# Kernel optimization log

Measured on AMD Instinct MI355X. Metric: run time of the kernel, lower is better.

## Reference

```python
import jax, jax.numpy as jnp
import numpy as np

N_NODES = 100000
N_EDGES = 1600000
NODE_F = 64
EDGE_F = 32
BN_EPS = 1e-5


def setup_inputs() -> dict:
    key = jax.random.key(0)
    ks = jax.random.split(key, 8)
    in_dim = 2 * NODE_F + EDGE_F  # 160
    scale = 1.0 / np.sqrt(in_dim)
    return {
        "node_attrs": jax.random.normal(ks[0], (N_NODES, NODE_F), jnp.float32),
        "edge_index": jax.random.randint(ks[1], (2, N_EDGES), 0, N_NODES, jnp.int64),
        "edge_attrs": jax.random.normal(ks[2], (N_EDGES, EDGE_F), jnp.float32),
        "W_f": jax.random.normal(ks[3], (in_dim, NODE_F), jnp.float32) * scale,
        "b_f": jnp.zeros((NODE_F,), jnp.float32),
        "W_s": jax.random.normal(ks[4], (in_dim, NODE_F), jnp.float32) * scale,
        "b_s": jnp.zeros((NODE_F,), jnp.float32),
        "gamma": jnp.ones((NODE_F,), jnp.float32),
        "beta": jnp.zeros((NODE_F,), jnp.float32),
    }


def reference(node_attrs, edge_index, edge_attrs, W_f, b_f, W_s, b_s, gamma, beta):
    source, target = edge_index[0], edge_index[1]
    x_i = node_attrs[source]            # [E, F] gather
    x_j = node_attrs[target]            # [E, F] gather
    z = jnp.concatenate([x_i, x_j, edge_attrs], axis=-1)  # [E, 2F+Fe]
    # gated MLP: sigmoid(lin_f(z)) * softplus(lin_s(z))
    h = jax.nn.sigmoid(z @ W_f + b_f) * jax.nn.softplus(z @ W_s + b_s)  # [E, F]
    # scatter-add messages to source nodes
    message = jax.ops.segment_sum(h, source, num_segments=node_attrs.shape[0])  # [N, F]
    # BatchNorm1d in training mode: batch stats over node dim (biased variance)
    mean = jnp.mean(message, axis=0)
    var = jnp.mean((message - mean) ** 2, axis=0)
    normed = (message - mean) * jax.lax.rsqrt(var + BN_EPS) * gamma + beta
    return node_attrs + normed
```

## Files before the change

### kernel.cpp

```cpp
#include <hip/hip_runtime.h>
#include <math.h>

#define N_NODES 100000
#define N_EDGES 1600000
#define NODE_F  64
#define IN_DIM  160
#define N_TILES 25000
#define ZSTRIDE 168
#define EDGE_GRID 1792

typedef __attribute__((ext_vector_type(8))) short short8;
typedef __attribute__((ext_vector_type(4))) float f32x4;

static __device__ inline unsigned short f2bf(float f) {
    union { float f; unsigned u; } v; v.f = f;
    unsigned r = v.u + 0x7fffu + ((v.u >> 16) & 1u);
    return (unsigned short)(r >> 16);
}

static __device__ inline unsigned pack2(float lo, float hi) {
    union { float f; unsigned u; } a, b; a.f = lo; b.f = hi;
    const unsigned ra = a.u + 0x7fffu + ((a.u >> 16) & 1u);
    const unsigned rb = b.u + 0x7fffu + ((b.u >> 16) & 1u);
    return __builtin_amdgcn_perm(rb, ra, 0x07060302u);
}

static __device__ __forceinline__ void tile_barrier() {
    __builtin_amdgcn_sched_barrier(0);
    asm volatile("s_waitcnt lgkmcnt(0)" ::: "memory");
    __builtin_amdgcn_s_barrier();
    __builtin_amdgcn_sched_barrier(0);
}

__global__ __launch_bounds__(256, 7) void edge_kernel(
    const float* __restrict__ node_attrs,
    const int*   __restrict__ edge_src,
    const int*   __restrict__ edge_tgt,
    const float* __restrict__ edge_attrs,
    const float* __restrict__ W_f, const float* __restrict__ b_f,
    const float* __restrict__ W_s, const float* __restrict__ b_s,
    float* __restrict__ msg)
{
    __shared__ __align__(16) short sbuf[64 * ZSTRIDE];
    unsigned* sbuf32 = (unsigned*)sbuf;

    const int tid  = threadIdx.x;
    const int wave = tid >> 6;
    const int lane = tid & 63;
    const int quad = lane >> 4;
    const int l15  = lane & 15;

    short8 bF[5], bS[5];
#pragma unroll
    for (int mat = 0; mat < 2; ++mat) {
        const float* W = mat ? W_s : W_f;
        __syncthreads();
        for (int idx = tid; idx < IN_DIM * 64; idx += 256) {
            const int k = idx >> 6, n = idx & 63;
            sbuf[n * ZSTRIDE + k] = (short)f2bf(W[idx]);
        }
        __syncthreads();
#pragma unroll
        for (int kc = 0; kc < 5; ++kc) {
            const short8 b = *(const short8*)&sbuf[(16 * wave + l15) * ZSTRIDE + kc * 32 + quad * 8];
            if (mat) bS[kc] = b; else bF[kc] = b;
        }
    }

    const float bias_f = b_f[16 * wave + l15];
    const float bias_s = b_s[16 * wave + l15];
    float* const msgf  = msg + 16 * wave + l15;

    int srcv = edge_src[blockIdx.x * 64 + lane];
    int tgtv = edge_tgt[blockIdx.x * 64 + lane];

    for (int t = blockIdx.x; t < N_TILES; t += EDGE_GRID) {
        const int e0 = t * 64;

        tile_barrier();

#pragma unroll
        for (int i = 0; i < 8; ++i) {
            const int el   = i * 2 + (quad >> 1);
            const int half = quad & 1;
            const int sl   = 16 * wave + el;
            const int ns   = __shfl(srcv, sl);
            const int nt   = __shfl(tgtv, sl);
            const int node = half ? nt : ns;
            const float4 v = *(const float4*)&node_attrs[node * 64 + l15 * 4];
            uint2 o; o.x = pack2(v.x, v.y); o.y = pack2(v.z, v.w);
            *(uint2*)&sbuf32[sl * (ZSTRIDE / 2) + half * 32 + l15 * 2] = o;
        }
#pragma unroll
        for (int i = 0; i < 2; ++i) {
            const int p  = i * 256 + tid;
            const int el = p >> 3, g = p & 7;
            const float4 v = *(const float4*)&edge_attrs[(size_t)(e0 + el) * 32 + g * 4];
            uint2 o; o.x = pack2(v.x, v.y); o.y = pack2(v.z, v.w);
            *(uint2*)&sbuf32[el * (ZSTRIDE / 2) + 64 + g * 2] = o;
        }

        const int tn = t + EDGE_GRID;
        int nsrc = 0, ntgt = 0;
        if (tn < N_TILES) {
            nsrc = edge_src[tn * 64 + lane];
            ntgt = edge_tgt[tn * 64 + lane];
        }
        tile_barrier();

#pragma unroll
        for (int mt = 0; mt < 4; ++mt) {
            f32x4 accF = {0.f, 0.f, 0.f, 0.f};
            f32x4 accS = {0.f, 0.f, 0.f, 0.f};
#pragma unroll
            for (int kc = 0; kc < 5; ++kc) {
                const short8 a = *(const short8*)&sbuf[(mt * 16 + l15) * ZSTRIDE + kc * 32 + quad * 8];
                accF = __builtin_amdgcn_mfma_f32_16x16x32_bf16(a, bF[kc], accF, 0, 0, 0);
                accS = __builtin_amdgcn_mfma_f32_16x16x32_bf16(a, bS[kc], accS, 0, 0, 0);
            }
#pragma unroll
            for (int r = 0; r < 4; ++r) {
                const float xf = accF[r] + bias_f;
                const float xs = accS[r] + bias_s;
                const float sig = __builtin_amdgcn_rcpf(1.0f + __expf(-xf));
                const float sp  = fmaxf(xs, 0.0f) + __logf(1.0f + __expf(-fabsf(xs)));
                const float h   = sig * sp;
                const int sl    = mt * 16 + quad * 4 + r;
                const int node  = __shfl(srcv, sl);
                atomicAdd(&msgf[node * 64], h);
            }
        }

        srcv = nsrc;
        tgtv = ntgt;
    }
}

#define STATS_BLOCKS 1024
__global__ __launch_bounds__(256) void stats_kernel(
    const float* __restrict__ msg, float* __restrict__ stats)
{
    const int tid = threadIdx.x;
    const int g4  = tid & 15;
    const int r0  = tid >> 4;
    float4 s = {0.f, 0.f, 0.f, 0.f};
    float4 q = {0.f, 0.f, 0.f, 0.f};
    for (int r = blockIdx.x * 16 + r0; r < N_NODES; r += STATS_BLOCKS * 16) {
        const float4 v = *(const float4*)&msg[(size_t)r * 64 + g4 * 4];
        s.x += v.x; s.y += v.y; s.z += v.z; s.w += v.w;
        q.x = fmaf(v.x, v.x, q.x);
        q.y = fmaf(v.y, v.y, q.y);
        q.z = fmaf(v.z, v.z, q.z);
        q.w = fmaf(v.w, v.w, q.w);
    }
    __shared__ float4 rs[256];
    __shared__ float4 rq[256];
    rs[tid] = s;
    rq[tid] = q;
    __syncthreads();
    if (tid < 16) {
        float4 S = rs[tid];
        float4 Q = rq[tid];
        for (int k = 1; k < 16; ++k) {
            const float4 a = rs[k * 16 + tid];
            const float4 b = rq[k * 16 + tid];
            S.x += a.x; S.y += a.y; S.z += a.z; S.w += a.w;
            Q.x += b.x; Q.y += b.y; Q.z += b.z; Q.w += b.w;
        }
        atomicAdd(&stats[tid * 4 + 0], S.x);
        atomicAdd(&stats[tid * 4 + 1], S.y);
        atomicAdd(&stats[tid * 4 + 2], S.z);
        atomicAdd(&stats[tid * 4 + 3], S.w);
        atomicAdd(&stats[64 + tid * 4 + 0], Q.x);
        atomicAdd(&stats[64 + tid * 4 + 1], Q.y);
        atomicAdd(&stats[64 + tid * 4 + 2], Q.z);
        atomicAdd(&stats[64 + tid * 4 + 3], Q.w);
    }
}

__global__ __launch_bounds__(256) void norm_kernel(
    const float* __restrict__ node_attrs,
    const float* __restrict__ stats,
    const float* __restrict__ gamma,
    const float* __restrict__ beta,
    float* __restrict__ out)
{
    const int i = blockIdx.x * blockDim.x + threadIdx.x;
    const int idx = i * 4;
    if (idx >= N_NODES * 64) return;
    const int f = idx & 63;
    const float inv_n = 1.0f / (float)N_NODES;

    const float4 m4 = *(const float4*)&out[idx];
    const float4 x4 = *(const float4*)&node_attrs[idx];

    float mean[4], rstd[4], gm[4], bt[4];
#pragma unroll
    for (int j = 0; j < 4; ++j) {
        mean[j] = stats[f + j] * inv_n;
        const float var = stats[64 + f + j] * inv_n - mean[j] * mean[j];
        rstd[j] = rsqrtf(var + 1e-5f);
        gm[j] = gamma[f + j];
        bt[j] = beta[f + j];
    }
    float4 o;
    o.x = x4.x + (m4.x - mean[0]) * rstd[0] * gm[0] + bt[0];
    o.y = x4.y + (m4.y - mean[1]) * rstd[1] * gm[1] + bt[1];
    o.z = x4.z + (m4.z - mean[2]) * rstd[2] * gm[2] + bt[2];
    o.w = x4.w + (m4.w - mean[3]) * rstd[3] * gm[3] + bt[3];
    *(float4*)&out[idx] = o;
}

extern "C" void kernel_launch(void* const* d_in, const int* in_sizes, int n_in,
                              void* d_out, int out_size, void* d_ws, size_t ws_size,
                              hipStream_t stream)
{
    const float* node_attrs = (const float*)d_in[0];
    const int*   edge_index = (const int*)d_in[1];
    const float* edge_attrs = (const float*)d_in[2];
    const float* W_f   = (const float*)d_in[3];
    const float* b_f   = (const float*)d_in[4];
    const float* W_s   = (const float*)d_in[5];
    const float* b_s   = (const float*)d_in[6];
    const float* gamma = (const float*)d_in[7];
    const float* beta  = (const float*)d_in[8];

    float* out   = (float*)d_out;
    float* stats = (float*)d_ws;

    const int* edge_src = edge_index;
    const int* edge_tgt = edge_index + N_EDGES;

    hipMemsetAsync(out, 0, (size_t)N_NODES * NODE_F * sizeof(float), stream);
    hipMemsetAsync(stats, 0, 128 * sizeof(float), stream);

    edge_kernel<<<EDGE_GRID, 256, 0, stream>>>(
        node_attrs, edge_src, edge_tgt, edge_attrs, W_f, b_f, W_s, b_s, out);

    stats_kernel<<<STATS_BLOCKS, 256, 0, stream>>>(out, stats);

    norm_kernel<<<(N_NODES * NODE_F / 4 + 255) / 256, 256, 0, stream>>>(
        node_attrs, stats, gamma, beta, out);
}
```

Before: 718.9 us.

## Fuse edge, stats and norm kernels into one persistent kernel with grid barriers

Merges the three kernels into a single persistent launch of 1536 blocks that uses atomic-counter grid barriers between the scatter, batch-stats and normalization phases. The aim is to remove launch gaps and the separate stats memset. The grid shrinks from 1792 to 1536 blocks with a launch-bounds occupancy of 6, and the custom LDS-only barrier is replaced by plain __syncthreads. The grid barrier needs every block to be resident at once and has a spin-timeout fallback, so it risks wrong results or stalls if residency is not guaranteed. The barriers also serialize the tail work.

```diff
diff --git a/kernel.cpp b/kernel.cpp
--- a/kernel.cpp
+++ b/kernel.cpp
@@ -7,7 +7,8 @@
 #define IN_DIM  160
 #define N_TILES 25000
 #define ZSTRIDE 168
-#define EDGE_GRID 1792
+#define GRID    1536
+#define BLOCK   256
 
 typedef __attribute__((ext_vector_type(8))) short short8;
 typedef __attribute__((ext_vector_type(4))) float f32x4;
@@ -25,21 +26,33 @@
     return __builtin_amdgcn_perm(rb, ra, 0x07060302u);
 }
 
-static __device__ __forceinline__ void tile_barrier() {
-    __builtin_amdgcn_sched_barrier(0);
-    asm volatile("s_waitcnt lgkmcnt(0)" ::: "memory");
-    __builtin_amdgcn_s_barrier();
-    __builtin_amdgcn_sched_barrier(0);
-}
-
-__global__ __launch_bounds__(256, 7) void edge_kernel(
+static __device__ __forceinline__ void grid_sync(int* ctr) {
+    __threadfence();
+    __syncthreads();
+    if (threadIdx.x == 0) {
+        __hip_atomic_fetch_add(ctr, 1, __ATOMIC_ACQ_REL, __HIP_MEMORY_SCOPE_AGENT);
+        int spins = 0;
+        while (__hip_atomic_load(ctr, __ATOMIC_ACQUIRE, __HIP_MEMORY_SCOPE_AGENT) < GRID) {
+            __builtin_amdgcn_s_sleep(8);
+            if (++spins > (1 << 22)) break;
+        }
+    }
+    __syncthreads();
+    __threadfence();
+}
+
+__global__ __launch_bounds__(BLOCK, 6) void fused_kernel(
     const float* __restrict__ node_attrs,
     const int*   __restrict__ edge_src,
     const int*   __restrict__ edge_tgt,
     const float* __restrict__ edge_attrs,
     const float* __restrict__ W_f, const float* __restrict__ b_f,
     const float* __restrict__ W_s, const float* __restrict__ b_s,
-    float* __restrict__ msg)
+    const float* __restrict__ gamma,
+    const float* __restrict__ beta,
+    float* __restrict__ out,
+    float* __restrict__ stats,
+    int*   __restrict__ ctr)
 {
     __shared__ __align__(16) short sbuf[64 * ZSTRIDE];
     unsigned* sbuf32 = (unsigned*)sbuf;
@@ -50,6 +63,7 @@
     const int quad = lane >> 4;
     const int l15  = lane & 15;
 
+
     short8 bF[5], bS[5];
 #pragma unroll
     for (int mat = 0; mat < 2; ++mat) {
@@ -69,15 +83,15 @@
 
     const float bias_f = b_f[16 * wave + l15];
     const float bias_s = b_s[16 * wave + l15];
-    float* const msgf  = msg + 16 * wave + l15;
+    float* const msgf  = out + 16 * wave + l15;
 
     int srcv = edge_src[blockIdx.x * 64 + lane];
     int tgtv = edge_tgt[blockIdx.x * 64 + lane];
 
-    for (int t = blockIdx.x; t < N_TILES; t += EDGE_GRID) {
+    for (int t = blockIdx.x; t < N_TILES; t += GRID) {
         const int e0 = t * 64;
 
-        tile_barrier();
+        __syncthreads();
 
 #pragma unroll
         for (int i = 0; i < 8; ++i) {
@@ -100,13 +114,13 @@
             *(uint2*)&sbuf32[el * (ZSTRIDE / 2) + 64 + g * 2] = o;
         }
 
-        const int tn = t + EDGE_GRID;
+        const int tn = t + GRID;
         int nsrc = 0, ntgt = 0;
         if (tn < N_TILES) {
             nsrc = edge_src[tn * 64 + lane];
             ntgt = edge_tgt[tn * 64 + lane];
         }
-        tile_barrier();
+        __syncthreads();
 
 #pragma unroll
         for (int mt = 0; mt < 4; ++mt) {
@@ -134,81 +148,77 @@
         srcv = nsrc;
         tgtv = ntgt;
     }
-}
-
-#define STATS_BLOCKS 1024
-__global__ __launch_bounds__(256) void stats_kernel(
-    const float* __restrict__ msg, float* __restrict__ stats)
-{
-    const int tid = threadIdx.x;
-    const int g4  = tid & 15;
-    const int r0  = tid >> 4;
-    float4 s = {0.f, 0.f, 0.f, 0.f};
-    float4 q = {0.f, 0.f, 0.f, 0.f};
-    for (int r = blockIdx.x * 16 + r0; r < N_NODES; r += STATS_BLOCKS * 16) {
-        const float4 v = *(const float4*)&msg[(size_t)r * 64 + g4 * 4];
-        s.x += v.x; s.y += v.y; s.z += v.z; s.w += v.w;
-        q.x = fmaf(v.x, v.x, q.x);
-        q.y = fmaf(v.y, v.y, q.y);
-        q.z = fmaf(v.z, v.z, q.z);
-        q.w = fmaf(v.w, v.w, q.w);
-    }
-    __shared__ float4 rs[256];
-    __shared__ float4 rq[256];
-    rs[tid] = s;
-    rq[tid] = q;
-    __syncthreads();
-    if (tid < 16) {
-        float4 S = rs[tid];
-        float4 Q = rq[tid];
-        for (int k = 1; k < 16; ++k) {
-            const float4 a = rs[k * 16 + tid];
-            const float4 b = rq[k * 16 + tid];
-            S.x += a.x; S.y += a.y; S.z += a.z; S.w += a.w;
-            Q.x += b.x; Q.y += b.y; Q.z += b.z; Q.w += b.w;
-        }
-        atomicAdd(&stats[tid * 4 + 0], S.x);
-        atomicAdd(&stats[tid * 4 + 1], S.y);
-        atomicAdd(&stats[tid * 4 + 2], S.z);
-        atomicAdd(&stats[tid * 4 + 3], S.w);
-        atomicAdd(&stats[64 + tid * 4 + 0], Q.x);
-        atomicAdd(&stats[64 + tid * 4 + 1], Q.y);
-        atomicAdd(&stats[64 + tid * 4 + 2], Q.z);
-        atomicAdd(&stats[64 + tid * 4 + 3], Q.w);
-    }
-}
-
-__global__ __launch_bounds__(256) void norm_kernel(
-    const float* __restrict__ node_attrs,
-    const float* __restrict__ stats,
-    const float* __restrict__ gamma,
-    const float* __restrict__ beta,
-    float* __restrict__ out)
-{
-    const int i = blockIdx.x * blockDim.x + threadIdx.x;
-    const int idx = i * 4;
-    if (idx >= N_NODES * 64) return;
-    const int f = idx & 63;
-    const float inv_n = 1.0f / (float)N_NODES;
-
-    const float4 m4 = *(const float4*)&out[idx];
-    const float4 x4 = *(const float4*)&node_attrs[idx];
-
-    float mean[4], rstd[4], gm[4], bt[4];
-#pragma unroll
-    for (int j = 0; j < 4; ++j) {
-        mean[j] = stats[f + j] * inv_n;
-        const float var = stats[64 + f + j] * inv_n - mean[j] * mean[j];
-        rstd[j] = rsqrtf(var + 1e-5f);
-        gm[j] = gamma[f + j];
-        bt[j] = beta[f + j];
-    }
-    float4 o;
-    o.x = x4.x + (m4.x - mean[0]) * rstd[0] * gm[0] + bt[0];
-    o.y = x4.y + (m4.y - mean[1]) * rstd[1] * gm[1] + bt[1];
-    o.z = x4.z + (m4.z - mean[2]) * rstd[2] * gm[2] + bt[2];
-    o.w = x4.w + (m4.w - mean[3]) * rstd[3] * gm[3] + bt[3];
-    *(float4*)&out[idx] = o;
+
+    grid_sync(&ctr[0]);
+
+    {
+        const int c  = tid & 15;
+        const int r0 = blockIdx.x * 16 + (tid >> 4);
+        float4 s = {0.f, 0.f, 0.f, 0.f};
+        float4 q = {0.f, 0.f, 0.f, 0.f};
+        for (int r = r0; r < N_NODES; r += GRID * 16) {
+            const float4 v = *(const float4*)&out[(size_t)r * 64 + c * 4];
+            s.x += v.x; s.y += v.y; s.z += v.z; s.w += v.w;
+            q.x = fmaf(v.x, v.x, q.x);
+            q.y = fmaf(v.y, v.y, q.y);
+            q.z = fmaf(v.z, v.z, q.z);
+            q.w = fmaf(v.w, v.w, q.w);
+        }
+        float4* rs = (float4*)sbuf;
+        float4* rq = rs + 256;
+        rs[tid] = s;
+        rq[tid] = q;
+        __syncthreads();
+        if (tid < 16) {
+            float4 S = rs[tid];
+            float4 Q = rq[tid];
+#pragma unroll
+            for (int k = 1; k < 16; ++k) {
+                const float4 a = rs[k * 16 + tid];
+                const float4 b = rq[k * 16 + tid];
+                S.x += a.x; S.y += a.y; S.z += a.z; S.w += a.w;
+                Q.x += b.x; Q.y += b.y; Q.z += b.z; Q.w += b.w;
+            }
+            atomicAdd(&stats[tid * 4 + 0], S.x);
+            atomicAdd(&stats[tid * 4 + 1], S.y);
+            atomicAdd(&stats[tid * 4 + 2], S.z);
+            atomicAdd(&stats[tid * 4 + 3], S.w);
+            atomicAdd(&stats[64 + tid * 4 + 0], Q.x);
+            atomicAdd(&stats[64 + tid * 4 + 1], Q.y);
+            atomicAdd(&stats[64 + tid * 4 + 2], Q.z);
+            atomicAdd(&stats[64 + tid * 4 + 3], Q.w);
+        }
+    }
+
+    grid_sync(&ctr[1]);
+
+    {
+        const float inv_n = 1.0f / (float)N_NODES;
+        const int g0 = blockIdx.x * BLOCK + tid;
+        for (int i = g0; i < N_NODES * NODE_F / 4; i += GRID * BLOCK) {
+            const int idx = i * 4;
+            const int f = idx & 63;
+
+            const float4 m4 = *(const float4*)&out[idx];
+            const float4 x4 = *(const float4*)&node_attrs[idx];
+
+            float mean[4], rstd[4], gm[4], bt[4];
+#pragma unroll
+            for (int j = 0; j < 4; ++j) {
+                mean[j] = stats[f + j] * inv_n;
+                const float var = stats[64 + f + j] * inv_n - mean[j] * mean[j];
+                rstd[j] = rsqrtf(var + 1e-5f);
+                gm[j] = gamma[f + j];
+                bt[j] = beta[f + j];
+            }
+            float4 o;
+            o.x = x4.x + (m4.x - mean[0]) * rstd[0] * gm[0] + bt[0];
+            o.y = x4.y + (m4.y - mean[1]) * rstd[1] * gm[1] + bt[1];
+            o.z = x4.z + (m4.z - mean[2]) * rstd[2] * gm[2] + bt[2];
+            o.w = x4.w + (m4.w - mean[3]) * rstd[3] * gm[3] + bt[3];
+            *(float4*)&out[idx] = o;
+        }
+    }
 }
 
 extern "C" void kernel_launch(void* const* d_in, const int* in_sizes, int n_in,
@@ -227,18 +237,15 @@
 
     float* out   = (float*)d_out;
     float* stats = (float*)d_ws;
+    int*   ctr   = (int*)((char*)d_ws + 512);
 
     const int* edge_src = edge_index;
     const int* edge_tgt = edge_index + N_EDGES;
 
     hipMemsetAsync(out, 0, (size_t)N_NODES * NODE_F * sizeof(float), stream);
-    hipMemsetAsync(stats, 0, 128 * sizeof(float), stream);
-
-    edge_kernel<<<EDGE_GRID, 256, 0, stream>>>(
-        node_attrs, edge_src, edge_tgt, edge_attrs, W_f, b_f, W_s, b_s, out);
-
-    stats_kernel<<<STATS_BLOCKS, 256, 0, stream>>>(out, stats);
-
-    norm_kernel<<<(N_NODES * NODE_F / 4 + 255) / 256, 256, 0, stream>>>(
-        node_attrs, stats, gamma, beta, out);
-}
+    hipMemsetAsync(d_ws, 0, 1024, stream);
+
+    fused_kernel<<<GRID, BLOCK, 0, stream>>>(
+        node_attrs, edge_src, edge_tgt, edge_attrs,
+        W_f, b_f, W_s, b_s, gamma, beta, out, stats, ctr);
+}
```

New measurement: 1.588 ms. +120.9%, slower.
